# Performance work log

Hardware: AMD Instinct MI355X
Metric: run time of the kernel (lower is better)

The kernel has to match this reference:

```python
import jax, jax.numpy as jnp
import numpy as np

H, DK, DV = 4, 64, 64        # heads, key/value head dims (hidden=256)
M, TOPK = 4, 2               # num memories, router top-k
GN, EPS, COND_SCALE = 16.0, 1e-5, 1.0


def setup_inputs() -> dict:
    key = jax.random.key(0)
    ks = jax.random.split(key, 12)
    B, Q, K, D = 8, 64, 256, 256
    w = lambda k, shape, fan: jax.random.normal(k, shape, jnp.float32) / np.sqrt(fan).astype(np.float32)
    return {
        "query": jax.random.normal(ks[0], (B, Q, D), jnp.float32),
        "keyval": jax.random.normal(ks[1], (B, K, D), jnp.float32),
        "attention_mask_kv": jnp.ones((B, K), jnp.int32),
        "W_cond": w(ks[2], (D, D), D),
        "W_q": w(ks[3], (D, H * DK), D),
        "W_k": w(ks[4], (D, H * DK), D),
        "W_v": w(ks[5], (D, H * DV), D),
        "W_gk1": w(ks[6], (D, 16), D),
        "W_gk2": w(ks[7], (16, H * DK), 16),
        "b_gk2": jnp.zeros((H * DK,), jnp.float32),
        "W_router": w(ks[8], (D, M), D),
        "norm_w": jnp.ones((DV,), jnp.float32),
        "W_o": w(ks[9], (H * DV, D), H * DV),
    }


def _mem_last(q_last, k, v, gk, sel, wgt):
    """Last-token output of one gated linear-attention memory.
    S_t = diag(exp(gk_t)) S_{t-1} + k_t v_t^T ; o_T = q_T S_T.
    q_last: (N,H,DK); k,gk: (N,K,H,DK); v: (N,K,H,DV); sel,wgt: (N,K)."""
    k_e = k * sel[:, :, None, None]
    v_e = v * wgt[:, :, None, None]
    gk_e = gk * sel[:, :, None, None]          # unselected tokens: no decay, no update
    G = jnp.cumsum(gk_e, axis=1)               # (N,K,H,DK), log decays
    decay = jnp.exp(G[:, -1:, :, :] - G)       # remaining decay to last step, <= 1
    s = jnp.einsum('nhd,nthd->nth', q_last, k_e * decay)
    return jnp.einsum('nth,nthv->nhv', s, v_e)


def reference(query, keyval, attention_mask_kv, W_cond, W_q, W_k, W_v,
              W_gk1, W_gk2, b_gk2, W_router, norm_w, W_o):
    B, Q, D = query.shape
    K = keyval.shape[1]
    N = B * Q
    # broadcast KV expansion + cond injection
    cond = (query @ W_cond) * COND_SCALE                         # (B,Q,D)
    x = (keyval[:, None, :, :] + cond[:, :, None, :]).reshape(N, K, D)
    m = jnp.broadcast_to(attention_mask_kv[:, None, :].astype(x.dtype), (B, Q, K)).reshape(N, K)
    # projections
    q = (x @ W_q).reshape(N, K, H, DK)
    k = (x @ W_k).reshape(N, K, H, DK) * m[:, :, None, None]
    v = (x @ W_v).reshape(N, K, H, DV) * m[:, :, None, None]
    gk = (jax.nn.log_sigmoid(x @ W_gk1 @ W_gk2 + b_gk2) / GN).reshape(N, K, H, DK)
    gk = gk * m[:, :, None, None]
    # router: softmax -> top-k -> renormalize
    router_logits = (x @ W_router).reshape(N * K, M)
    probs = jax.nn.softmax(router_logits, axis=-1)
    topv, topi = jax.lax.top_k(probs, TOPK)
    topv = topv / jnp.sum(topv, axis=-1, keepdims=True)
    w_mem = jnp.sum(jax.nn.one_hot(topi, M, dtype=x.dtype) * topv[..., None], axis=-2)
    w_mem = w_mem.reshape(N, K, M)
    # shared memory (always on) + routed memories
    q_last = q[:, -1]
    ones = jnp.ones((N, K), x.dtype)
    o = _mem_last(q_last, k, v, gk, ones, ones)
    for e in range(M):
        we = w_mem[:, :, e]
        o = o + _mem_last(q_last, k, v, gk, (we > 0).astype(x.dtype), we)
    # per-head RMSNorm + output projection
    o = o * jax.lax.rsqrt(jnp.mean(o * o, axis=-1, keepdims=True) + EPS) * norm_w
    out = (o.reshape(N, H * DV) @ W_o).reshape(B, Q, D)
    return out, router_logits
```

## Files before the change

kernel.cpp:

```cpp
#include <hip/hip_runtime.h>
#include <math.h>

#define Hh   4
#define Bb   8
#define Qq   64
#define Kk   256
#define Dd   256
#define Nn   (Bb * Qq)
#define GNf  16.0f
#define EPSf 1e-5f
#define WB   1088

__device__ __forceinline__ float wred(float x) {
#pragma unroll
    for (int off = 32; off > 0; off >>= 1)
        x += __shfl_xor(x, off, 64);
    return x;
}

__global__ __launch_bounds__(256) void pack_wb(
    const float* __restrict__ Wq, const float* __restrict__ Wk,
    const float* __restrict__ Wv, const float* __restrict__ Wg1,
    const float* __restrict__ Wg2, const float* __restrict__ Wr,
    float* __restrict__ Wb)
{
    const int idx = blockIdx.x * 256 + threadIdx.x;
    const int k = idx / WB, j = idx % WB;
    float v;
    if (j < 256)       v = Wq[(size_t)k * 256 + j];
    else if (j < 512)  v = Wk[(size_t)k * 256 + j - 256];
    else if (j < 768)  v = Wv[(size_t)k * 256 + j - 512];
    else if (j < 1024) {
        const int c = j - 768;
        float s = 0.f;
#pragma unroll
        for (int i = 0; i < 16; ++i)
            s = fmaf(Wg1[(size_t)k * 16 + i], Wg2[(size_t)i * 256 + c], s);
        v = s;
    }
    else if (j < 1028) v = Wr[(size_t)k * 4 + (j - 1024)];
    else               v = 0.f;
    Wb[idx] = v;
}

__global__ __launch_bounds__(256) void gemm1(
    const float* __restrict__ keyval, const float* __restrict__ query,
    const float* __restrict__ Wb, const float* __restrict__ W_cond,
    float* __restrict__ KVb, float* __restrict__ cond)
{
    __shared__ float As[64][17];
    __shared__ float Ws[16][65];
    const int tid = threadIdx.x;

    int id = blockIdx.x;
    const float* A; const float* Bp; float* C;
    int ldb, ldc;
    if (id < 544) {
        const int bm = (id / 17) * 64, bn = (id % 17) * 64;
        A  = keyval + (size_t)bm * Dd;
        Bp = Wb + bn;        ldb = WB;
        C  = KVb + (size_t)bm * WB + bn;  ldc = WB;
    } else {
        id -= 544;
        const int bm = (id >> 2) * 64, bn = (id & 3) * 64;
        A  = query + (size_t)bm * Dd;
        Bp = W_cond + bn;    ldb = Dd;
        C  = cond + (size_t)bm * Dd + bn; ldc = Dd;
    }

    const int ty = tid >> 4, tx = tid & 15;
    const int aRow = tid >> 2, aCol = (tid & 3) * 4;
    const int wRow = tid >> 6, wCol = tid & 63;

    float acc[4][4] = {};

    for (int k0 = 0; k0 < Dd; k0 += 16) {
        const float4 av = *(const float4*)(A + (size_t)aRow * Dd + k0 + aCol);
        As[aRow][aCol + 0] = av.x;
        As[aRow][aCol + 1] = av.y;
        As[aRow][aCol + 2] = av.z;
        As[aRow][aCol + 3] = av.w;
#pragma unroll
        for (int r = 0; r < 4; ++r)
            Ws[wRow + 4 * r][wCol] = Bp[(size_t)(k0 + wRow + 4 * r) * ldb + wCol];
        __syncthreads();
#pragma unroll
        for (int kk = 0; kk < 16; ++kk) {
            float a[4], wv[4];
#pragma unroll
            for (int i = 0; i < 4; ++i) a[i] = As[ty * 4 + i][kk];
#pragma unroll
            for (int j = 0; j < 4; ++j) wv[j] = Ws[kk][tx * 4 + j];
#pragma unroll
            for (int i = 0; i < 4; ++i)
#pragma unroll
                for (int j = 0; j < 4; ++j)
                    acc[i][j] = fmaf(a[i], wv[j], acc[i][j]);
        }
        __syncthreads();
    }

#pragma unroll
    for (int i = 0; i < 4; ++i)
#pragma unroll
        for (int j = 0; j < 4; ++j)
            C[(size_t)(ty * 4 + i) * ldc + tx * 4 + j] = acc[i][j];
}

__global__ __launch_bounds__(256) void gemm2(
    const float* __restrict__ cond, const float* __restrict__ Wb,
    float* __restrict__ Cb)
{
    __shared__ float As[64][17];
    __shared__ float Ws[16][65];
    const int tid = threadIdx.x;
    const int bm = blockIdx.y * 64;
    const int bn = blockIdx.x * 64;
    const int ty = tid >> 4, tx = tid & 15;
    const int aRow = tid >> 2, aCol = (tid & 3) * 4;
    const int wRow = tid >> 6, wCol = tid & 63;

    float acc[4][4] = {};

    for (int k0 = 0; k0 < Dd; k0 += 16) {
        const float4 av = *(const float4*)(cond + (size_t)(bm + aRow) * Dd + k0 + aCol);
        As[aRow][aCol + 0] = av.x;
        As[aRow][aCol + 1] = av.y;
        As[aRow][aCol + 2] = av.z;
        As[aRow][aCol + 3] = av.w;
#pragma unroll
        for (int r = 0; r < 4; ++r)
            Ws[wRow + 4 * r][wCol] = Wb[(size_t)(k0 + wRow + 4 * r) * WB + bn + wCol];
        __syncthreads();
#pragma unroll
        for (int kk = 0; kk < 16; ++kk) {
            float a[4], wv[4];
#pragma unroll
            for (int i = 0; i < 4; ++i) a[i] = As[ty * 4 + i][kk];
#pragma unroll
            for (int j = 0; j < 4; ++j) wv[j] = Ws[kk][tx * 4 + j];
#pragma unroll
            for (int i = 0; i < 4; ++i)
#pragma unroll
                for (int j = 0; j < 4; ++j)
                    acc[i][j] = fmaf(a[i], wv[j], acc[i][j]);
        }
        __syncthreads();
    }

#pragma unroll
    for (int i = 0; i < 4; ++i)
#pragma unroll
        for (int j = 0; j < 4; ++j)
            Cb[(size_t)(bm + ty * 4 + i) * WB + bn + tx * 4 + j] = acc[i][j];
}

__global__ __launch_bounds__(256) void mom_fused(
    const float* __restrict__ KVb, const float* __restrict__ Cb,
    const float* __restrict__ b_gk2, const int* __restrict__ mask,
    const float* __restrict__ W_o, const float* __restrict__ norm_w,
    float* __restrict__ out, float* __restrict__ logits)
{
    __shared__ float4 wm[Kk];
    __shared__ float  Ptile[4][16][68];
    __shared__ float  sbuf[4][16];
    __shared__ float  onorm[Dd];

    const int n = blockIdx.x;
    const int b = n >> 6;
    const int j = threadIdx.x;
    const int lane = j & 63;
    const int wv = j >> 6;

    const float qc = Cb[(size_t)n * WB + j];
    const float kc = Cb[(size_t)n * WB + 256 + j];
    const float vc = Cb[(size_t)n * WB + 512 + j];
    const float pc = Cb[(size_t)n * WB + 768 + j] + b_gk2[j];
    const float4 rc = *(const float4*)(Cb + (size_t)n * WB + 1024);

    {
        const float4 kvr = *(const float4*)(KVb + (size_t)(b * Kk + j) * WB + 1024);
        float l[4] = {kvr.x + rc.x, kvr.y + rc.y, kvr.z + rc.z, kvr.w + rc.w};
        *(float4*)(logits + ((size_t)n * Kk + j) * 4) = make_float4(l[0], l[1], l[2], l[3]);

        int i1 = 0;
#pragma unroll
        for (int q = 1; q < 4; ++q) if (l[q] > l[i1]) i1 = q;
        int i2 = -1;
#pragma unroll
        for (int q = 0; q < 4; ++q) {
            if (q == i1) continue;
            if (i2 < 0 || l[q] > l[i2]) i2 = q;
        }
        const float mx = fmaxf(l[i1], l[i2]);
        const float e1 = __expf(l[i1] - mx);
        const float e2 = __expf(l[i2] - mx);
        const float inv = 1.f / (e1 + e2);
        float w[4] = {0.f, 0.f, 0.f, 0.f};
        w[i1] = e1 * inv;
        w[i2] = e2 * inv;
        wm[j] = make_float4(w[0], w[1], w[2], w[3]);
    }
    __syncthreads();

    const float ql = KVb[(size_t)(b * Kk + Kk - 1) * WB + j] + qc;
    const float* pk = KVb + (size_t)b * Kk * WB + 256 + j;
    const float* pv = KVb + (size_t)b * Kk * WB + 512 + j;
    const float* pp = KVb + (size_t)b * Kk * WB + 768 + j;
    const int*   pm = mask + b * Kk;

    float E0 = 1.f, E1 = 1.f, E2 = 1.f, E3 = 1.f, E4 = 1.f;
    float o = 0.f;
    const int tl = lane & 15, qq = lane >> 4;

    for (int t0 = Kk - 16; t0 >= 0; t0 -= 16) {
        float vreg[16];
#pragma unroll
        for (int i = 0; i < 16; ++i) {
            const int t = t0 + 15 - i;
            const float mf  = (float)pm[t];
            const float kk  = (pk[(size_t)t * WB] + kc) * mf;
            const float vvv = (pv[(size_t)t * WB] + vc) * mf;
            const float pre = pp[(size_t)t * WB] + pc;
            const float4 w  = wm[t];

            const float ls = fminf(pre, 0.f) - __logf(1.f + __expf(-fabsf(pre)));
            float dg = __expf(ls * (1.0f / GNf));
            dg = (mf != 0.f) ? dg : 1.f;

            const float zf = E0 + w.x * E1 + w.y * E2 + w.z * E3 + w.w * E4;
            Ptile[wv][i][lane] = ql * kk * zf;
            vreg[i] = vvv;

            E0 *= dg;
            E1 *= (w.x > 0.f) ? dg : 1.f;
            E2 *= (w.y > 0.f) ? dg : 1.f;
            E3 *= (w.z > 0.f) ? dg : 1.f;
            E4 *= (w.w > 0.f) ? dg : 1.f;
        }
        __builtin_amdgcn_wave_barrier();

        float s = 0.f;
#pragma unroll
        for (int r = 0; r < 4; ++r) {
            const float4 p4 = *(const float4*)&Ptile[wv][tl][qq * 16 + r * 4];
            s += (p4.x + p4.y) + (p4.z + p4.w);
        }
        s += __shfl_xor(s, 16, 64);
        s += __shfl_xor(s, 32, 64);
        sbuf[wv][tl] = s;
        __builtin_amdgcn_wave_barrier();
#pragma unroll
        for (int r = 0; r < 4; ++r) {
            const float4 sv = *(const float4*)&sbuf[wv][r * 4];
            o = fmaf(sv.x, vreg[r * 4 + 0], o);
            o = fmaf(sv.y, vreg[r * 4 + 1], o);
            o = fmaf(sv.z, vreg[r * 4 + 2], o);
            o = fmaf(sv.w, vreg[r * 4 + 3], o);
        }
    }

    const float ms = wred(o * o) * (1.0f / 64.0f);
    onorm[j] = o * rsqrtf(ms + EPSf) * norm_w[lane];
    __syncthreads();

    float acc = 0.f;
#pragma unroll 8
    for (int k = 0; k < Dd; ++k)
        acc = fmaf(onorm[k], W_o[(size_t)k * Dd + j], acc);
    out[(size_t)n * Dd + j] = acc;
}

extern "C" void kernel_launch(void* const* d_in, const int* in_sizes, int n_in,
                              void* d_out, int out_size, void* d_ws, size_t ws_size,
                              hipStream_t stream)
{
    const float* query    = (const float*)d_in[0];
    const float* keyval   = (const float*)d_in[1];
    const int*   mask     = (const int*)  d_in[2];
    const float* W_cond   = (const float*)d_in[3];
    const float* W_q      = (const float*)d_in[4];
    const float* W_k      = (const float*)d_in[5];
    const float* W_v      = (const float*)d_in[6];
    const float* W_gk1    = (const float*)d_in[7];
    const float* W_gk2    = (const float*)d_in[8];
    const float* b_gk2    = (const float*)d_in[9];
    const float* W_router = (const float*)d_in[10];
    const float* norm_w   = (const float*)d_in[11];
    const float* W_o      = (const float*)d_in[12];

    float* out    = (float*)d_out;
    float* logits = out + Nn * Dd;

    float* p = (float*)d_ws;
    float* Wb   = p; p += Dd * WB;
    float* KVb  = p; p += Bb * Kk * WB;
    float* cond = p; p += Nn * Dd;
    float* Cb   = p; p += Nn * WB;

    pack_wb<<<(Dd * WB) / 256, dim3(256), 0, stream>>>(
        W_q, W_k, W_v, W_gk1, W_gk2, W_router, Wb);

    gemm1<<<576, dim3(256), 0, stream>>>(keyval, query, Wb, W_cond, KVb, cond);

    gemm2<<<dim3(WB / 64, Nn / 64), dim3(256), 0, stream>>>(cond, Wb, Cb);

    mom_fused<<<Nn, dim3(256), 0, stream>>>(
        KVb, Cb, b_gk2, mask, W_o, norm_w, out, logits);
}
```

Baseline: 196.8 us.

## Interleave k/v/gate projections as float4, enlarge GEMM tiles, double-buffer scan loads

The projection GEMMs now write the key, value and gate columns (and q in gemm2) interleaved per channel, so the recurrent scan reads one float4 per timestep instead of three strided floats. The query projection of keyval is limited to the last token per batch, computed by a dedicated block, which skips the q-columns for all other tokens. GEMM tiles grow to 128x64 with 8x4 register blocking. The scan kernel double-buffers 16-step chunks in registers and sets occupancy launch bounds. Fewer GEMM blocks and higher register pressure may reduce parallelism.

```diff
diff --git a/kernel.cpp b/kernel.cpp
--- a/kernel.cpp
+++ b/kernel.cpp
@@ -1,13 +1,12 @@
 #include <hip/hip_runtime.h>
 #include <math.h>
 
-#define Hh   4
 #define Bb   8
 #define Qq   64
 #define Kk   256
 #define Dd   256
 #define Nn   (Bb * Qq)
-#define GNf  16.0f
+#define GNi  0.0625f
 #define EPSf 1e-5f
 #define WB   1088
 
@@ -43,122 +42,197 @@
     Wb[idx] = v;
 }
 
+__device__ __forceinline__ void gemm_core(
+    const float* __restrict__ A, const float* __restrict__ Bm, int ldb,
+    float (&acc)[8][4], float* As, float* Ws)
+{
+    const int tid = threadIdx.x;
+    const int r  = tid >> 1;
+    const int kl = (tid & 1) * 8;
+    const int wc = tid & 63;
+    const int kr = (tid >> 6) * 4;
+    const int ty = tid >> 4;
+    const int tx = tid & 15;
+
+    for (int k0 = 0; k0 < Dd; k0 += 16) {
+        const float4 a0 = *(const float4*)(A + (size_t)r * Dd + k0 + kl);
+        const float4 a1 = *(const float4*)(A + (size_t)r * Dd + k0 + kl + 4);
+        As[(kl + 0) * 132 + r] = a0.x;
+        As[(kl + 1) * 132 + r] = a0.y;
+        As[(kl + 2) * 132 + r] = a0.z;
+        As[(kl + 3) * 132 + r] = a0.w;
+        As[(kl + 4) * 132 + r] = a1.x;
+        As[(kl + 5) * 132 + r] = a1.y;
+        As[(kl + 6) * 132 + r] = a1.z;
+        As[(kl + 7) * 132 + r] = a1.w;
+#pragma unroll
+        for (int u = 0; u < 4; ++u)
+            Ws[(kr + u) * 68 + wc] = Bm[(size_t)(k0 + kr + u) * ldb + wc];
+        __syncthreads();
+#pragma unroll
+        for (int kk = 0; kk < 16; ++kk) {
+            const float4 aL = *(const float4*)&As[kk * 132 + ty * 8];
+            const float4 aH = *(const float4*)&As[kk * 132 + ty * 8 + 4];
+            const float4 bv = *(const float4*)&Ws[kk * 68 + tx * 4];
+            const float av[8] = {aL.x, aL.y, aL.z, aL.w, aH.x, aH.y, aH.z, aH.w};
+            const float bw[4] = {bv.x, bv.y, bv.z, bv.w};
+#pragma unroll
+            for (int i = 0; i < 8; ++i)
+#pragma unroll
+                for (int j = 0; j < 4; ++j)
+                    acc[i][j] = fmaf(av[i], bw[j], acc[i][j]);
+        }
+        __syncthreads();
+    }
+}
+
 __global__ __launch_bounds__(256) void gemm1(
     const float* __restrict__ keyval, const float* __restrict__ query,
     const float* __restrict__ Wb, const float* __restrict__ W_cond,
-    float* __restrict__ KVb, float* __restrict__ cond)
-{
-    __shared__ float As[64][17];
-    __shared__ float Ws[16][65];
+    float* __restrict__ KVi, float* __restrict__ KVr,
+    float* __restrict__ cond, float* __restrict__ KVq8)
+{
+    __shared__ float As[16 * 132];
+    __shared__ float Ws[16 * 68];
+    const int id = blockIdx.x;
     const int tid = threadIdx.x;
 
-    int id = blockIdx.x;
-    const float* A; const float* Bp; float* C;
-    int ldb, ldc;
-    if (id < 544) {
-        const int bm = (id / 17) * 64, bn = (id % 17) * 64;
-        A  = keyval + (size_t)bm * Dd;
-        Bp = Wb + bn;        ldb = WB;
-        C  = KVb + (size_t)bm * WB + bn;  ldc = WB;
+    if (id == 224) {
+        for (int b8 = 0; b8 < 8; ++b8)
+            As[b8 * 256 + tid] = keyval[((size_t)b8 * Kk + 255) * Dd + tid];
+        __syncthreads();
+        float acc8[8] = {};
+        for (int k = 0; k < 256; ++k) {
+            const float wq = Wb[(size_t)k * WB + tid];
+#pragma unroll
+            for (int b8 = 0; b8 < 8; ++b8)
+                acc8[b8] = fmaf(As[b8 * 256 + k], wq, acc8[b8]);
+        }
+        for (int b8 = 0; b8 < 8; ++b8)
+            KVq8[b8 * 256 + tid] = acc8[b8];
+        return;
+    }
+
+    float acc[8][4] = {};
+    const int ty = tid >> 4, tx = tid & 15;
+
+    if (id < 208) {
+        const int bm  = (id / 13) * 128;
+        const int bnA = 256 + (id % 13) * 64;
+        gemm_core(keyval + (size_t)bm * Dd, Wb + bnA, WB, acc, As, Ws);
+        if (bnA < 1024) {
+            const int reg = (bnA >> 8) - 1;
+            const int cb  = bnA & 255;
+#pragma unroll
+            for (int i = 0; i < 8; ++i) {
+                const size_t rowo = (size_t)(bm + ty * 8 + i) * 1024;
+#pragma unroll
+                for (int jj = 0; jj < 4; ++jj)
+                    KVi[rowo + (size_t)(cb + tx * 4 + jj) * 4 + reg] = acc[i][jj];
+            }
+        } else if (tx == 0) {
+#pragma unroll
+            for (int i = 0; i < 8; ++i)
+                *(float4*)&KVr[(size_t)(bm + ty * 8 + i) * 4] =
+                    make_float4(acc[i][0], acc[i][1], acc[i][2], acc[i][3]);
+        }
     } else {
-        id -= 544;
-        const int bm = (id >> 2) * 64, bn = (id & 3) * 64;
-        A  = query + (size_t)bm * Dd;
-        Bp = W_cond + bn;    ldb = Dd;
-        C  = cond + (size_t)bm * Dd + bn; ldc = Dd;
-    }
-
-    const int ty = tid >> 4, tx = tid & 15;
-    const int aRow = tid >> 2, aCol = (tid & 3) * 4;
-    const int wRow = tid >> 6, wCol = tid & 63;
-
-    float acc[4][4] = {};
-
-    for (int k0 = 0; k0 < Dd; k0 += 16) {
-        const float4 av = *(const float4*)(A + (size_t)aRow * Dd + k0 + aCol);
-        As[aRow][aCol + 0] = av.x;
-        As[aRow][aCol + 1] = av.y;
-        As[aRow][aCol + 2] = av.z;
-        As[aRow][aCol + 3] = av.w;
-#pragma unroll
-        for (int r = 0; r < 4; ++r)
-            Ws[wRow + 4 * r][wCol] = Bp[(size_t)(k0 + wRow + 4 * r) * ldb + wCol];
-        __syncthreads();
-#pragma unroll
-        for (int kk = 0; kk < 16; ++kk) {
-            float a[4], wv[4];
-#pragma unroll
-            for (int i = 0; i < 4; ++i) a[i] = As[ty * 4 + i][kk];
-#pragma unroll
-            for (int j = 0; j < 4; ++j) wv[j] = Ws[kk][tx * 4 + j];
-#pragma unroll
-            for (int i = 0; i < 4; ++i)
-#pragma unroll
-                for (int j = 0; j < 4; ++j)
-                    acc[i][j] = fmaf(a[i], wv[j], acc[i][j]);
-        }
-        __syncthreads();
-    }
-
-#pragma unroll
-    for (int i = 0; i < 4; ++i)
-#pragma unroll
-        for (int j = 0; j < 4; ++j)
-            C[(size_t)(ty * 4 + i) * ldc + tx * 4 + j] = acc[i][j];
+        const int id2 = id - 208;
+        const int bm = (id2 >> 2) * 128;
+        const int bn = (id2 & 3) * 64;
+        gemm_core(query + (size_t)bm * Dd, W_cond + bn, Dd, acc, As, Ws);
+#pragma unroll
+        for (int i = 0; i < 8; ++i)
+            *(float4*)&cond[(size_t)(bm + ty * 8 + i) * Dd + bn + tx * 4] =
+                make_float4(acc[i][0], acc[i][1], acc[i][2], acc[i][3]);
+    }
 }
 
 __global__ __launch_bounds__(256) void gemm2(
     const float* __restrict__ cond, const float* __restrict__ Wb,
-    float* __restrict__ Cb)
-{
-    __shared__ float As[64][17];
-    __shared__ float Ws[16][65];
+    float* __restrict__ Cbi, float* __restrict__ Cr)
+{
+    __shared__ float As[16 * 132];
+    __shared__ float Ws[16 * 68];
+    const int id = blockIdx.x;
     const int tid = threadIdx.x;
-    const int bm = blockIdx.y * 64;
-    const int bn = blockIdx.x * 64;
+    const int bm = (id / 17) * 128;
+    const int bn = (id % 17) * 64;
+    float acc[8][4] = {};
+    gemm_core(cond + (size_t)bm * Dd, Wb + bn, WB, acc, As, Ws);
     const int ty = tid >> 4, tx = tid & 15;
-    const int aRow = tid >> 2, aCol = (tid & 3) * 4;
-    const int wRow = tid >> 6, wCol = tid & 63;
-
-    float acc[4][4] = {};
-
-    for (int k0 = 0; k0 < Dd; k0 += 16) {
-        const float4 av = *(const float4*)(cond + (size_t)(bm + aRow) * Dd + k0 + aCol);
-        As[aRow][aCol + 0] = av.x;
-        As[aRow][aCol + 1] = av.y;
-        As[aRow][aCol + 2] = av.z;
-        As[aRow][aCol + 3] = av.w;
-#pragma unroll
-        for (int r = 0; r < 4; ++r)
-            Ws[wRow + 4 * r][wCol] = Wb[(size_t)(k0 + wRow + 4 * r) * WB + bn + wCol];
-        __syncthreads();
-#pragma unroll
-        for (int kk = 0; kk < 16; ++kk) {
-            float a[4], wv[4];
-#pragma unroll
-            for (int i = 0; i < 4; ++i) a[i] = As[ty * 4 + i][kk];
-#pragma unroll
-            for (int j = 0; j < 4; ++j) wv[j] = Ws[kk][tx * 4 + j];
-#pragma unroll
-            for (int i = 0; i < 4; ++i)
-#pragma unroll
-                for (int j = 0; j < 4; ++j)
-                    acc[i][j] = fmaf(a[i], wv[j], acc[i][j]);
-        }
-        __syncthreads();
-    }
-
-#pragma unroll
-    for (int i = 0; i < 4; ++i)
-#pragma unroll
-        for (int j = 0; j < 4; ++j)
-            Cb[(size_t)(bm + ty * 4 + i) * WB + bn + tx * 4 + j] = acc[i][j];
-}
-
-__global__ __launch_bounds__(256) void mom_fused(
-    const float* __restrict__ KVb, const float* __restrict__ Cb,
-    const float* __restrict__ b_gk2, const int* __restrict__ mask,
-    const float* __restrict__ W_o, const float* __restrict__ norm_w,
+    if (bn < 1024) {
+        const int reg = bn >> 8;
+        const int cb  = bn & 255;
+#pragma unroll
+        for (int i = 0; i < 8; ++i) {
+            const size_t rowo = (size_t)(bm + ty * 8 + i) * 1024;
+#pragma unroll
+            for (int jj = 0; jj < 4; ++jj)
+                Cbi[rowo + (size_t)(cb + tx * 4 + jj) * 4 + reg] = acc[i][jj];
+        }
+    } else if (tx == 0) {
+#pragma unroll
+        for (int i = 0; i < 8; ++i)
+            *(float4*)&Cr[(size_t)(bm + ty * 8 + i) * 4] =
+                make_float4(acc[i][0], acc[i][1], acc[i][2], acc[i][3]);
+    }
+}
+
+__device__ __forceinline__ void tile_step(
+    const float4* buf, int t0, const int* __restrict__ pm, const float4* wm,
+    float ql, float kc, float vc, float pc,
+    float& E0, float& E1, float& E2, float& E3, float& E4, float& o,
+    float (*Pt)[68], float* sb, int lane, int tl, int qq)
+{
+    float vreg[16];
+#pragma unroll
+    for (int i = 0; i < 16; ++i) {
+        const int t = t0 + 15 - i;
+        const float mf = (float)pm[t];
+        const float4 kv = buf[i];
+        const float kkv = (kv.x + kc) * mf;
+        vreg[i] = (kv.y + vc) * mf;
+        const float pre = kv.z + pc;
+        const float4 w = wm[t];
+        const float ls = fminf(pre, 0.f) - __logf(1.f + __expf(-fabsf(pre)));
+        float dg = __expf(ls * GNi);
+        dg = (mf != 0.f) ? dg : 1.f;
+        const float zf = E0 + w.x * E1 + w.y * E2 + w.z * E3 + w.w * E4;
+        Pt[i][lane] = ql * kkv * zf;
+        E0 *= dg;
+        E1 *= (w.x > 0.f) ? dg : 1.f;
+        E2 *= (w.y > 0.f) ? dg : 1.f;
+        E3 *= (w.z > 0.f) ? dg : 1.f;
+        E4 *= (w.w > 0.f) ? dg : 1.f;
+    }
+    __builtin_amdgcn_wave_barrier();
+    float s = 0.f;
+#pragma unroll
+    for (int r = 0; r < 4; ++r) {
+        const float4 p4 = *(const float4*)&Pt[tl][qq * 16 + r * 4];
+        s += (p4.x + p4.y) + (p4.z + p4.w);
+    }
+    s += __shfl_xor(s, 16, 64);
+    s += __shfl_xor(s, 32, 64);
+    sb[tl] = s;
+    __builtin_amdgcn_wave_barrier();
+#pragma unroll
+    for (int r = 0; r < 4; ++r) {
+        const float4 sv = *(const float4*)&sb[r * 4];
+        o = fmaf(sv.x, vreg[r * 4 + 0], o);
+        o = fmaf(sv.y, vreg[r * 4 + 1], o);
+        o = fmaf(sv.z, vreg[r * 4 + 2], o);
+        o = fmaf(sv.w, vreg[r * 4 + 3], o);
+    }
+}
+
+__global__ __launch_bounds__(256, 2) void mom_fused(
+    const float4* __restrict__ KVi, const float* __restrict__ KVr,
+    const float4* __restrict__ Cbi, const float* __restrict__ Cr,
+    const float* __restrict__ KVq8, const float* __restrict__ b_gk2,
+    const int* __restrict__ mask, const float* __restrict__ W_o,
+    const float* __restrict__ norm_w,
     float* __restrict__ out, float* __restrict__ logits)
 {
     __shared__ float4 wm[Kk];
@@ -172,16 +246,17 @@
     const int lane = j & 63;
     const int wv = j >> 6;
 
-    const float qc = Cb[(size_t)n * WB + j];
-    const float kc = Cb[(size_t)n * WB + 256 + j];
-    const float vc = Cb[(size_t)n * WB + 512 + j];
-    const float pc = Cb[(size_t)n * WB + 768 + j] + b_gk2[j];
-    const float4 rc = *(const float4*)(Cb + (size_t)n * WB + 1024);
+    const float4 c4 = Cbi[(size_t)n * 256 + j];
+    const float qc = c4.x, kc = c4.y, vc = c4.z;
+    const float pc = c4.w + b_gk2[j];
+    const float ql = KVq8[b * 256 + j] + qc;
 
     {
-        const float4 kvr = *(const float4*)(KVb + (size_t)(b * Kk + j) * WB + 1024);
-        float l[4] = {kvr.x + rc.x, kvr.y + rc.y, kvr.z + rc.z, kvr.w + rc.w};
-        *(float4*)(logits + ((size_t)n * Kk + j) * 4) = make_float4(l[0], l[1], l[2], l[3]);
+        const float4 kvr = *(const float4*)&KVr[(size_t)(b * Kk + j) * 4];
+        const float4 cr  = *(const float4*)&Cr[(size_t)n * 4];
+        float l[4] = {kvr.x + cr.x, kvr.y + cr.y, kvr.z + cr.z, kvr.w + cr.w};
+        *(float4*)(logits + ((size_t)n * Kk + j) * 4) =
+            make_float4(l[0], l[1], l[2], l[3]);
 
         int i1 = 0;
 #pragma unroll
@@ -203,61 +278,31 @@
     }
     __syncthreads();
 
-    const float ql = KVb[(size_t)(b * Kk + Kk - 1) * WB + j] + qc;
-    const float* pk = KVb + (size_t)b * Kk * WB + 256 + j;
-    const float* pv = KVb + (size_t)b * Kk * WB + 512 + j;
-    const float* pp = KVb + (size_t)b * Kk * WB + 768 + j;
-    const int*   pm = mask + b * Kk;
+    const float4* pkv = KVi + (size_t)b * Kk * 256 + j;
+    const int*    pm  = mask + b * Kk;
 
     float E0 = 1.f, E1 = 1.f, E2 = 1.f, E3 = 1.f, E4 = 1.f;
     float o = 0.f;
     const int tl = lane & 15, qq = lane >> 4;
 
-    for (int t0 = Kk - 16; t0 >= 0; t0 -= 16) {
-        float vreg[16];
-#pragma unroll
-        for (int i = 0; i < 16; ++i) {
-            const int t = t0 + 15 - i;
-            const float mf  = (float)pm[t];
-            const float kk  = (pk[(size_t)t * WB] + kc) * mf;
-            const float vvv = (pv[(size_t)t * WB] + vc) * mf;
-            const float pre = pp[(size_t)t * WB] + pc;
-            const float4 w  = wm[t];
-
-            const float ls = fminf(pre, 0.f) - __logf(1.f + __expf(-fabsf(pre)));
-            float dg = __expf(ls * (1.0f / GNf));
-            dg = (mf != 0.f) ? dg : 1.f;
-
-            const float zf = E0 + w.x * E1 + w.y * E2 + w.z * E3 + w.w * E4;
-            Ptile[wv][i][lane] = ql * kk * zf;
-            vreg[i] = vvv;
-
-            E0 *= dg;
-            E1 *= (w.x > 0.f) ? dg : 1.f;
-            E2 *= (w.y > 0.f) ? dg : 1.f;
-            E3 *= (w.z > 0.f) ? dg : 1.f;
-            E4 *= (w.w > 0.f) ? dg : 1.f;
-        }
-        __builtin_amdgcn_wave_barrier();
-
-        float s = 0.f;
-#pragma unroll
-        for (int r = 0; r < 4; ++r) {
-            const float4 p4 = *(const float4*)&Ptile[wv][tl][qq * 16 + r * 4];
-            s += (p4.x + p4.y) + (p4.z + p4.w);
-        }
-        s += __shfl_xor(s, 16, 64);
-        s += __shfl_xor(s, 32, 64);
-        sbuf[wv][tl] = s;
-        __builtin_amdgcn_wave_barrier();
-#pragma unroll
-        for (int r = 0; r < 4; ++r) {
-            const float4 sv = *(const float4*)&sbuf[wv][r * 4];
-            o = fmaf(sv.x, vreg[r * 4 + 0], o);
-            o = fmaf(sv.y, vreg[r * 4 + 1], o);
-            o = fmaf(sv.z, vreg[r * 4 + 2], o);
-            o = fmaf(sv.w, vreg[r * 4 + 3], o);
-        }
+    float4 bufA[16], bufB[16];
+#pragma unroll
+    for (int i = 0; i < 16; ++i) bufA[i] = pkv[(size_t)(255 - i) * 256];
+
+    for (int pp = 0; pp < 8; ++pp) {
+        const int tA = 240 - 32 * pp;
+        const int tB = tA - 16;
+#pragma unroll
+        for (int i = 0; i < 16; ++i) bufB[i] = pkv[(size_t)(tB + 15 - i) * 256];
+        tile_step(bufA, tA, pm, wm, ql, kc, vc, pc,
+                  E0, E1, E2, E3, E4, o, Ptile[wv], sbuf[wv], lane, tl, qq);
+        if (pp < 7) {
+#pragma unroll
+            for (int i = 0; i < 16; ++i)
+                bufA[i] = pkv[(size_t)(tB - 16 + 15 - i) * 256];
+        }
+        tile_step(bufB, tB, pm, wm, ql, kc, vc, pc,
+                  E0, E1, E2, E3, E4, o, Ptile[wv], sbuf[wv], lane, tl, qq);
     }
 
     const float ms = wred(o * o) * (1.0f / 64.0f);
@@ -294,17 +339,22 @@
 
     float* p = (float*)d_ws;
     float* Wb   = p; p += Dd * WB;
-    float* KVb  = p; p += Bb * Kk * WB;
+    float* KVi  = p; p += (size_t)Bb * Kk * 1024;
+    float* KVr  = p; p += Bb * Kk * 4;
     float* cond = p; p += Nn * Dd;
-    float* Cb   = p; p += Nn * WB;
+    float* Cbi  = p; p += (size_t)Nn * 1024;
+    float* Cr   = p; p += Nn * 4;
+    float* KVq8 = p; p += Bb * Dd;
 
     pack_wb<<<(Dd * WB) / 256, dim3(256), 0, stream>>>(
         W_q, W_k, W_v, W_gk1, W_gk2, W_router, Wb);
 
-    gemm1<<<576, dim3(256), 0, stream>>>(keyval, query, Wb, W_cond, KVb, cond);
-
-    gemm2<<<dim3(WB / 64, Nn / 64), dim3(256), 0, stream>>>(cond, Wb, Cb);
+    gemm1<<<225, dim3(256), 0, stream>>>(
+        keyval, query, Wb, W_cond, KVi, KVr, cond, KVq8);
+
+    gemm2<<<68, dim3(256), 0, stream>>>(cond, Wb, Cbi, Cr);
 
     mom_fused<<<Nn, dim3(256), 0, stream>>>(
-        KVb, Cb, b_gk2, mask, W_o, norm_w, out, logits);
-}
+        (const float4*)KVi, KVr, (const float4*)Cbi, Cr,
+        KVq8, b_gk2, mask, W_o, norm_w, out, logits);
+}
```

Result: slower. 208.0 us (+5.7%).
